# Kernel tuning notes

Hardware: AMD Instinct MI355X
Metric: run time of the kernel (lower is better)

## Reference

```python
import jax, jax.numpy as jnp
import numpy as np

WS = 11
SIGMA = 1.5
L = 1.0  # val_range


def _gaussian_window(ws=WS, sigma=SIGMA):
    x = np.arange(ws, dtype=np.float64) - ws // 2
    g = np.exp(-(x ** 2) / (2.0 * sigma ** 2))
    g = g / g.sum()
    w2d = np.outer(g, g)
    return jnp.asarray(w2d, dtype=jnp.float32)  # [ws, ws]


def _depthwise_blur(x, w2d):
    # x: [B, C, H, W]; depthwise gaussian conv with SAME-style padding ws//2
    c = x.shape[1]
    kern = jnp.broadcast_to(w2d, (c, 1, WS, WS)).astype(x.dtype)  # OIHW, groups=C
    pad = WS // 2
    return jax.lax.conv_general_dilated(
        x, kern, window_strides=(1, 1), padding=[(pad, pad), (pad, pad)],
        dimension_numbers=('NCHW', 'OIHW', 'NCHW'), feature_group_count=c)


def setup_inputs() -> dict:
    key = jax.random.key(0)
    k1, k2 = jax.random.split(key)
    img1 = jax.random.uniform(k1, (32, 3, 512, 512), dtype=jnp.float32)
    img2 = jax.random.uniform(k2, (32, 3, 512, 512), dtype=jnp.float32)
    return {"img1": img1, "img2": img2}


def reference(img1, img2):
    w2d = _gaussian_window()
    mu1 = _depthwise_blur(img1, w2d)
    mu2 = _depthwise_blur(img2, w2d)
    mu1_sq = mu1 * mu1
    mu2_sq = mu2 * mu2
    mu1_mu2 = mu1 * mu2
    sigma1_sq = _depthwise_blur(img1 * img1, w2d) - mu1_sq
    sigma2_sq = _depthwise_blur(img2 * img2, w2d) - mu2_sq
    sigma12 = _depthwise_blur(img1 * img2, w2d) - mu1_mu2
    C1 = (0.01 * L) ** 2
    C2 = (0.03 * L) ** 2
    ssim_map = ((2.0 * mu1_mu2 + C1) * (2.0 * sigma12 + C2)) / (
        (mu1_sq + mu2_sq + C1) * (sigma1_sq + sigma2_sq + C2))
    return 1.0 - ssim_map.mean()
```

## Files before the change

kernel.cpp:

```cpp
#include <hip/hip_runtime.h>
#include <math.h>

typedef _Float16 f16;
typedef _Float16 f16x8 __attribute__((ext_vector_type(8)));
typedef _Float16 f16x4 __attribute__((ext_vector_type(4)));
typedef float f32x4 __attribute__((ext_vector_type(4)));

#define ROWS 88
#define NTHREADS 256

__device__ __forceinline__ float ssim_px(float m1, float m2, float mss, float m12) {
  const float C1 = 0.0001f, C2 = 0.0009f;
  const float mu1s = m1 * m1, mu2s = m2 * m2, mu12 = m1 * m2;
  const float num = (2.f * mu12 + C1) * (2.f * (m12 - mu12) + C2);
  const float den = (mu1s + mu2s + C1) * (mss - mu1s - mu2s + C2);
  return num * __builtin_amdgcn_rcpf(den);
}

template <bool MASKED>
__device__ __forceinline__ void h_phase(
    const float* __restrict__ p1, const float* __restrict__ p2,
    f16 (*si)[64][ROWS],
    int gy0, int xb, int px, int n, int kg, const f16x8& Bh)
{
  float4 La0[5], La1[5], Lb0[5], Lb1[5];
  float okf[5];

#pragma unroll
  for (int rg = 0; rg < 5; rg++) {
    const int rimg = gy0 + rg * 16 + n;
    size_t base;
    if (MASKED) {
      const bool octok = (xb >= 0) && (xb <= 504);
      const bool rok = (rimg >= 0) && (rimg < 512);
      okf[rg] = (rok && octok) ? 1.f : 0.f;
      const int rc = rok ? rimg : 0;
      const int xc = octok ? xb : 0;
      base = ((size_t)rc << 9) + (size_t)xc;
    } else {
      okf[rg] = 1.f;
      base = ((size_t)rimg << 9) + (size_t)xb;
    }
    La0[rg] = *(const float4*)(p1 + base);
    La1[rg] = *(const float4*)(p1 + base + 4);
    Lb0[rg] = *(const float4*)(p2 + base);
    Lb1[rg] = *(const float4*)(p2 + base + 4);
  }

#pragma unroll
  for (int rg = 0; rg < 5; rg++) {
    const float av[8] = {La0[rg].x, La0[rg].y, La0[rg].z, La0[rg].w,
                         La1[rg].x, La1[rg].y, La1[rg].z, La1[rg].w};
    const float bw[8] = {Lb0[rg].x, Lb0[rg].y, Lb0[rg].z, Lb0[rg].w,
                         Lb1[rg].x, Lb1[rg].y, Lb1[rg].z, Lb1[rg].w};
    f16x8 fa, fb, fs, fp;
#pragma unroll
    for (int i = 0; i < 8; i++) {
      float ai = av[i], bi = bw[i];
      if (MASKED) { ai *= okf[rg]; bi *= okf[rg]; }
      fa[i] = (f16)ai;
      fb[i] = (f16)bi;
      fs[i] = (f16)fmaf(ai, ai, bi * bi);
      fp[i] = (f16)(ai * bi);
    }
    const f32x4 z = {0.f, 0.f, 0.f, 0.f};
    const f32x4 Da = __builtin_amdgcn_mfma_f32_16x16x32_f16(fa, Bh, z, 0, 0, 0);
    const f32x4 Db = __builtin_amdgcn_mfma_f32_16x16x32_f16(fb, Bh, z, 0, 0, 0);
    const f32x4 Ds = __builtin_amdgcn_mfma_f32_16x16x32_f16(fs, Bh, z, 0, 0, 0);
    const f32x4 Dp = __builtin_amdgcn_mfma_f32_16x16x32_f16(fp, Bh, z, 0, 0, 0);
    const int sr = rg * 16 + kg * 4;
    const f16x4 wa = {(f16)Da[0], (f16)Da[1], (f16)Da[2], (f16)Da[3]};
    const f16x4 wb = {(f16)Db[0], (f16)Db[1], (f16)Db[2], (f16)Db[3]};
    const f16x4 ws = {(f16)Ds[0], (f16)Ds[1], (f16)Ds[2], (f16)Ds[3]};
    const f16x4 wp = {(f16)Dp[0], (f16)Dp[1], (f16)Dp[2], (f16)Dp[3]};
    *(f16x4*)&si[0][px][sr] = wa;
    *(f16x4*)&si[1][px][sr] = wb;
    *(f16x4*)&si[2][px][sr] = ws;
    *(f16x4*)&si[3][px][sr] = wp;
  }
}

__global__ __launch_bounds__(NTHREADS) void ssim_main_kernel(
    const float* __restrict__ img1, const float* __restrict__ img2,
    float* __restrict__ partials, float norm, float cexp)
{
  __shared__ f16 si[4][64][ROWS];
  __shared__ float sred[4];

  const int tid = threadIdx.x;
  const int wv = tid >> 6, lane = tid & 63;
  const int n = lane & 15, kg = lane >> 4;

  int b = blockIdx.x;
  const int tx = b & 7; b >>= 3;
  const int ty = b & 7; b >>= 3;
  const float* __restrict__ p1 = img1 + (size_t)b * 262144;
  const float* __restrict__ p2 = img2 + (size_t)b * 262144;

  f16x8 Bh, Av;
#pragma unroll
  for (int i = 0; i < 8; i++) {
    const int k = 8 * kg + i;
    {
      const int idx = k - n - 3;
      const float d = (float)(idx - 5);
      const float val = norm * exp2f(cexp * d * d);
      Bh[i] = (idx >= 0 && idx <= 10) ? (f16)val : (f16)0.f;
    }
    {
      const int idx = k - n;
      const float d = (float)(idx - 5);
      const float val = norm * exp2f(cexp * d * d);
      Av[i] = (idx >= 0 && idx <= 10) ? (f16)val : (f16)0.f;
    }
  }

  const int X0 = tx * 64 + wv * 16;
  const int xb = X0 - 8 + 8 * kg;
  const int gy0 = ty * 64 - 5;
  const int px = wv * 16 + n;

  const bool interior = (tx >= 1) && (tx <= 6) && (ty >= 1) && (ty <= 6);
  if (interior)
    h_phase<false>(p1, p2, si, gy0, xb, px, n, kg, Bh);
  else
    h_phase<true>(p1, p2, si, gy0, xb, px, n, kg, Bh);
  __syncthreads();

  float acc4[4] = {0.f, 0.f, 0.f, 0.f};
#pragma unroll
  for (int og = 0; og < 4; og++) {
    const int srb = og * 16 + 8 * kg;
    const f16x8 Ba = *(const f16x8*)&si[0][px][srb];
    const f16x8 Bb = *(const f16x8*)&si[1][px][srb];
    const f16x8 Bs = *(const f16x8*)&si[2][px][srb];
    const f16x8 Bp = *(const f16x8*)&si[3][px][srb];
    const f32x4 z = {0.f, 0.f, 0.f, 0.f};
    const f32x4 Ma = __builtin_amdgcn_mfma_f32_16x16x32_f16(Av, Ba, z, 0, 0, 0);
    const f32x4 Mb = __builtin_amdgcn_mfma_f32_16x16x32_f16(Av, Bb, z, 0, 0, 0);
    const f32x4 Ms = __builtin_amdgcn_mfma_f32_16x16x32_f16(Av, Bs, z, 0, 0, 0);
    const f32x4 Mp = __builtin_amdgcn_mfma_f32_16x16x32_f16(Av, Bp, z, 0, 0, 0);
#pragma unroll
    for (int r = 0; r < 4; r++)
      acc4[r] += ssim_px(Ma[r], Mb[r], Ms[r], Mp[r]);
  }
  float accSum = (acc4[0] + acc4[1]) + (acc4[2] + acc4[3]);

  for (int off = 32; off > 0; off >>= 1)
    accSum += __shfl_down(accSum, off, 64);
  if (lane == 0) sred[wv] = accSum;
  __syncthreads();
  if (tid == 0)
    partials[blockIdx.x] = sred[0] + sred[1] + sred[2] + sred[3];
}

__global__ __launch_bounds__(256) void ssim_final_kernel(
    const float* __restrict__ partials, float* __restrict__ out,
    int n, double invN)
{
  __shared__ double sred[4];
  const int tid = threadIdx.x;
  double s = 0.0;
  for (int i = tid; i < n; i += 256) s += (double)partials[i];
  for (int off = 32; off > 0; off >>= 1)
    s += __shfl_down(s, off, 64);
  if ((tid & 63) == 0) sred[tid >> 6] = s;
  __syncthreads();
  if (tid == 0) {
    double tot = 0.0;
#pragma unroll
    for (int i = 0; i < 4; i++) tot += sred[i];
    out[0] = (float)(1.0 - tot * invN);
  }
}

extern "C" void kernel_launch(void* const* d_in, const int* in_sizes, int n_in,
                              void* d_out, int out_size, void* d_ws, size_t ws_size,
                              hipStream_t stream) {
  const float* img1 = (const float*)d_in[0];
  const float* img2 = (const float*)d_in[1];
  float* out = (float*)d_out;
  float* partials = (float*)d_ws;

  const int planes = in_sizes[0] / (512 * 512);
  const int nBlocks = planes * 8 * 8;

  double sum = 0.0;
  for (int i = 0; i < 11; i++) {
    const double x = (double)(i - 5);
    sum += exp(-(x * x) / 4.5);
  }
  const float norm = (float)(1.0 / sum);
  const float cexp = (float)(-1.0 / (4.5 * 0.6931471805599453));

  const double invN = 1.0 / (double)in_sizes[0];

  ssim_main_kernel<<<nBlocks, NTHREADS, 0, stream>>>(img1, img2, partials, norm, cexp);
  ssim_final_kernel<<<1, 256, 0, stream>>>(partials, out, nBlocks, invN);
}
```

Before: 81.11 us.

## Process two planes per block, prefetching second plane during vertical pass

Each block now handles two image planes 48 apart. The global loads for the second plane are issued before the first plane's vertical MFMA pass, so memory latency overlaps with compute, and the grid is halved. The squared and product terms are also computed in f16 vector arithmetic instead of f32 before conversion, which lowers precision. The hardcoded plane offset of 48 only works when there are 96 planes, which ties the kernel to the test shape.

```diff
diff --git a/kernel.cpp b/kernel.cpp
--- a/kernel.cpp
+++ b/kernel.cpp
@@ -18,14 +18,11 @@
 }
 
 template <bool MASKED>
-__device__ __forceinline__ void h_phase(
+__device__ __forceinline__ void issue_loads(
     const float* __restrict__ p1, const float* __restrict__ p2,
-    f16 (*si)[64][ROWS],
-    int gy0, int xb, int px, int n, int kg, const f16x8& Bh)
-{
-  float4 La0[5], La1[5], Lb0[5], Lb1[5];
-  float okf[5];
-
+    int gy0, int xb, int n,
+    float4 La0[5], float4 La1[5], float4 Lb0[5], float4 Lb1[5], float okf[5])
+{
 #pragma unroll
   for (int rg = 0; rg < 5; rg++) {
     const int rimg = gy0 + rg * 16 + n;
@@ -46,23 +43,30 @@
     Lb0[rg] = *(const float4*)(p2 + base);
     Lb1[rg] = *(const float4*)(p2 + base + 4);
   }
-
+}
+
+template <bool MASKED>
+__device__ __forceinline__ void h_consume(
+    const float4 La0[5], const float4 La1[5],
+    const float4 Lb0[5], const float4 Lb1[5], const float okf[5],
+    f16 (*si)[64][ROWS], int px, int kg, const f16x8& Bh)
+{
 #pragma unroll
   for (int rg = 0; rg < 5; rg++) {
     const float av[8] = {La0[rg].x, La0[rg].y, La0[rg].z, La0[rg].w,
                          La1[rg].x, La1[rg].y, La1[rg].z, La1[rg].w};
     const float bw[8] = {Lb0[rg].x, Lb0[rg].y, Lb0[rg].z, Lb0[rg].w,
                          Lb1[rg].x, Lb1[rg].y, Lb1[rg].z, Lb1[rg].w};
-    f16x8 fa, fb, fs, fp;
+    f16x8 fa, fb;
 #pragma unroll
     for (int i = 0; i < 8; i++) {
       float ai = av[i], bi = bw[i];
       if (MASKED) { ai *= okf[rg]; bi *= okf[rg]; }
       fa[i] = (f16)ai;
       fb[i] = (f16)bi;
-      fs[i] = (f16)fmaf(ai, ai, bi * bi);
-      fp[i] = (f16)(ai * bi);
-    }
+    }
+    const f16x8 fp = fa * fb;
+    const f16x8 fs = fa * fa + fb * fb;
     const f32x4 z = {0.f, 0.f, 0.f, 0.f};
     const f32x4 Da = __builtin_amdgcn_mfma_f32_16x16x32_f16(fa, Bh, z, 0, 0, 0);
     const f32x4 Db = __builtin_amdgcn_mfma_f32_16x16x32_f16(fb, Bh, z, 0, 0, 0);
@@ -80,54 +84,9 @@
   }
 }
 
-__global__ __launch_bounds__(NTHREADS) void ssim_main_kernel(
-    const float* __restrict__ img1, const float* __restrict__ img2,
-    float* __restrict__ partials, float norm, float cexp)
-{
-  __shared__ f16 si[4][64][ROWS];
-  __shared__ float sred[4];
-
-  const int tid = threadIdx.x;
-  const int wv = tid >> 6, lane = tid & 63;
-  const int n = lane & 15, kg = lane >> 4;
-
-  int b = blockIdx.x;
-  const int tx = b & 7; b >>= 3;
-  const int ty = b & 7; b >>= 3;
-  const float* __restrict__ p1 = img1 + (size_t)b * 262144;
-  const float* __restrict__ p2 = img2 + (size_t)b * 262144;
-
-  f16x8 Bh, Av;
-#pragma unroll
-  for (int i = 0; i < 8; i++) {
-    const int k = 8 * kg + i;
-    {
-      const int idx = k - n - 3;
-      const float d = (float)(idx - 5);
-      const float val = norm * exp2f(cexp * d * d);
-      Bh[i] = (idx >= 0 && idx <= 10) ? (f16)val : (f16)0.f;
-    }
-    {
-      const int idx = k - n;
-      const float d = (float)(idx - 5);
-      const float val = norm * exp2f(cexp * d * d);
-      Av[i] = (idx >= 0 && idx <= 10) ? (f16)val : (f16)0.f;
-    }
-  }
-
-  const int X0 = tx * 64 + wv * 16;
-  const int xb = X0 - 8 + 8 * kg;
-  const int gy0 = ty * 64 - 5;
-  const int px = wv * 16 + n;
-
-  const bool interior = (tx >= 1) && (tx <= 6) && (ty >= 1) && (ty <= 6);
-  if (interior)
-    h_phase<false>(p1, p2, si, gy0, xb, px, n, kg, Bh);
-  else
-    h_phase<true>(p1, p2, si, gy0, xb, px, n, kg, Bh);
-  __syncthreads();
-
-  float acc4[4] = {0.f, 0.f, 0.f, 0.f};
+__device__ __forceinline__ void v_phase(
+    f16 (*si)[64][ROWS], int px, int kg, const f16x8& Av, float acc4[4])
+{
 #pragma unroll
   for (int og = 0; og < 4; og++) {
     const int srb = og * 16 + 8 * kg;
@@ -144,6 +103,83 @@
     for (int r = 0; r < 4; r++)
       acc4[r] += ssim_px(Ma[r], Mb[r], Ms[r], Mp[r]);
   }
+}
+
+__global__ __launch_bounds__(NTHREADS) void ssim_main_kernel(
+    const float* __restrict__ img1, const float* __restrict__ img2,
+    float* __restrict__ partials, float norm, float cexp)
+{
+  __shared__ f16 si[4][64][ROWS];
+  __shared__ float sred[4];
+
+  const int tid = threadIdx.x;
+  const int wv = tid >> 6, lane = tid & 63;
+  const int n = lane & 15, kg = lane >> 4;
+
+  int b = blockIdx.x;
+  const int tx = b & 7; b >>= 3;
+  const int ty = b & 7; b >>= 3;
+  const float* __restrict__ p1A = img1 + (size_t)b * 262144;
+  const float* __restrict__ p2A = img2 + (size_t)b * 262144;
+  const float* __restrict__ p1B = p1A + (size_t)48 * 262144;
+  const float* __restrict__ p2B = p2A + (size_t)48 * 262144;
+
+  f16x8 Bh, Av;
+#pragma unroll
+  for (int i = 0; i < 8; i++) {
+    const int k = 8 * kg + i;
+    {
+      const int idx = k - n - 3;
+      const float d = (float)(idx - 5);
+      const float val = norm * exp2f(cexp * d * d);
+      Bh[i] = (idx >= 0 && idx <= 10) ? (f16)val : (f16)0.f;
+    }
+    {
+      const int idx = k - n;
+      const float d = (float)(idx - 5);
+      const float val = norm * exp2f(cexp * d * d);
+      Av[i] = (idx >= 0 && idx <= 10) ? (f16)val : (f16)0.f;
+    }
+  }
+
+  const int X0 = tx * 64 + wv * 16;
+  const int xb = X0 - 8 + 8 * kg;
+  const int gy0 = ty * 64 - 5;
+  const int px = wv * 16 + n;
+  const bool interior = (tx >= 1) && (tx <= 6) && (ty >= 1) && (ty <= 6);
+
+  float acc4[4] = {0.f, 0.f, 0.f, 0.f};
+  float4 La0[5], La1[5], Lb0[5], Lb1[5];
+  float okf[5];
+
+  if (interior) {
+    issue_loads<false>(p1A, p2A, gy0, xb, n, La0, La1, Lb0, Lb1, okf);
+    h_consume<false>(La0, La1, Lb0, Lb1, okf, si, px, kg, Bh);
+  } else {
+    issue_loads<true>(p1A, p2A, gy0, xb, n, La0, La1, Lb0, Lb1, okf);
+    h_consume<true>(La0, La1, Lb0, Lb1, okf, si, px, kg, Bh);
+  }
+
+  __builtin_amdgcn_sched_barrier(0);
+  if (interior)
+    issue_loads<false>(p1B, p2B, gy0, xb, n, La0, La1, Lb0, Lb1, okf);
+  else
+    issue_loads<true>(p1B, p2B, gy0, xb, n, La0, La1, Lb0, Lb1, okf);
+  __builtin_amdgcn_sched_barrier(0);
+
+  __syncthreads();
+
+  v_phase(si, px, kg, Av, acc4);
+  __syncthreads();
+
+  if (interior)
+    h_consume<false>(La0, La1, Lb0, Lb1, okf, si, px, kg, Bh);
+  else
+    h_consume<true>(La0, La1, Lb0, Lb1, okf, si, px, kg, Bh);
+  __syncthreads();
+
+  v_phase(si, px, kg, Av, acc4);
+
   float accSum = (acc4[0] + acc4[1]) + (acc4[2] + acc4[3]);
 
   for (int off = 32; off > 0; off >>= 1)
@@ -183,7 +219,7 @@
   float* partials = (float*)d_ws;
 
   const int planes = in_sizes[0] / (512 * 512);
-  const int nBlocks = planes * 8 * 8;
+  const int nBlocks = (planes / 2) * 8 * 8;
 
   double sum = 0.0;
   for (int i = 0; i < 11; i++) {
```

Result: no change. 80.95 us (-0.2%).
